# Kernel tuning notes

Hardware: AMD Instinct MI355X
Metric: run time of the kernel (lower is better)

The kernel has to match this reference:

```python
import jax, jax.numpy as jnp
import numpy as np

N_NODES = 100000
N_GRAPHS = 1000
NPG = 100           # nodes per graph (fixed)
N_EDGES = 3200000   # avg degree 32
F_IN = 128
K = 30              # SortAggregation k
N_CLASSES = 10


def setup_inputs() -> dict:
    key = jax.random.key(0)
    ks = jax.random.split(key, 24)
    x = jax.random.normal(ks[0], (N_NODES, F_IN), jnp.float32)
    # edges constrained within each 100-node graph
    g = jax.random.randint(ks[1], (N_EDGES,), 0, N_GRAPHS)
    src = g * NPG + jax.random.randint(ks[2], (N_EDGES,), 0, NPG)
    dst = g * NPG + jax.random.randint(ks[3], (N_EDGES,), 0, NPG)
    edge_index = jnp.stack([src, dst]).astype(jnp.int32)
    batch = jnp.repeat(jnp.arange(N_GRAPHS, dtype=jnp.int32), NPG)

    def lin(k, fi, fo):
        return jax.random.normal(k, (fi, fo), jnp.float32) / np.sqrt(fi)

    return {
        "x": x, "edge_index": edge_index, "batch": batch,
        "W1": lin(ks[4], F_IN, 32), "b1": jnp.zeros((32,), jnp.float32),
        "W2": lin(ks[5], 32, 32),   "b2": jnp.zeros((32,), jnp.float32),
        "W3": lin(ks[6], 32, 32),   "b3": jnp.zeros((32,), jnp.float32),
        "W4": lin(ks[7], 32, 1),    "b4": jnp.zeros((1,), jnp.float32),
        "conv5_w": jax.random.normal(ks[8], (16, 1, 97), jnp.float32) / np.sqrt(97.0),
        "conv5_b": jnp.zeros((16,), jnp.float32),
        "conv6_w": jax.random.normal(ks[9], (32, 16, 5), jnp.float32) / np.sqrt(16 * 5.0),
        "conv6_b": jnp.zeros((32,), jnp.float32),
        "fc1_w": lin(ks[10], 352, 128), "fc1_b": jnp.zeros((128,), jnp.float32),
        "fc2_w": lin(ks[11], 128, N_CLASSES), "fc2_b": jnp.zeros((N_CLASSES,), jnp.float32),
    }


def reference(x, edge_index, batch,
              W1, b1, W2, b2, W3, b3, W4, b4,
              conv5_w, conv5_b, conv6_w, conv6_b,
              fc1_w, fc1_b, fc2_w, fc2_b):
    N = x.shape[0]
    src, dst = edge_index[0], edge_index[1]
    # remove_self_loops -> zero edge weight; GCNConv then re-adds self loops (weight 1)
    w = jnp.where(src == dst, 0.0, 1.0).astype(x.dtype)
    deg = jax.ops.segment_sum(w, dst, num_segments=N) + 1.0  # includes self loop
    dis = jax.lax.rsqrt(deg)
    norm = w * dis[src] * dis[dst]        # per-edge D^-1/2 A D^-1/2
    self_norm = dis * dis                 # self-loop coefficient 1/deg

    def gcn(h, W, b):
        h = h @ W                                   # [N, out]
        agg = jax.ops.segment_sum(norm[:, None] * h[src], dst, num_segments=N)
        return agg + self_norm[:, None] * h + b

    x1 = jnp.tanh(gcn(x, W1, b1))
    x2 = jnp.tanh(gcn(x1, W2, b2))
    x3 = jnp.tanh(gcn(x2, W3, b3))
    x4 = jnp.tanh(gcn(x3, W4, b4))
    h = jnp.concatenate([x1, x2, x3, x4], axis=-1)  # [N, 97]
    C = h.shape[-1]

    # SortAggregation(k=30): per graph, sort nodes by last channel descending, keep top k
    xs = h.reshape(N_GRAPHS, NPG, C)
    order = jnp.argsort(-xs[..., -1], axis=1)[:, :K]            # [B, K]
    pooled = jnp.take_along_axis(xs, order[:, :, None], axis=1)  # [B, K, C]
    y = pooled.reshape(N_GRAPHS, 1, K * C)                       # [B, 1, 2910]

    dn = ('NCH', 'OIH', 'NCH')
    y = jax.lax.conv_general_dilated(y, conv5_w, (97,), 'VALID', dimension_numbers=dn)
    y = jax.nn.relu(y + conv5_b[None, :, None])                  # [B, 16, 30]
    B, Co, L = y.shape
    y = y.reshape(B, Co, L // 2, 2).max(axis=-1)                 # maxpool(2,2) -> [B,16,15]
    y = jax.lax.conv_general_dilated(y, conv6_w, (1,), 'VALID', dimension_numbers=dn)
    y = jax.nn.relu(y + conv6_b[None, :, None])                  # [B, 32, 11]
    y = y.reshape(B, -1)                                         # [B, 352]
    out = jax.nn.relu(y @ fc1_w + fc1_b)                         # dropout = identity (eval)
    return jax.nn.log_softmax(out @ fc2_w + fc2_b, axis=-1)
```

## Files before the change

kernel.cpp:

```cpp
#include <hip/hip_runtime.h>

#define N_GRAPHS_C 1000
#define NPG_C      100
#define N_EDGES_C  3200000
#define KTOP_C     30
#define CAP        4096
#define NB_BUCKET  391

typedef _Float16 f16x8 __attribute__((ext_vector_type(8)));
typedef float    f32x4 __attribute__((ext_vector_type(4)));

__device__ __forceinline__ unsigned packh2(float x, float y) {
    _Float16 hx = (_Float16)x, hy = (_Float16)y;
    return (unsigned)__builtin_bit_cast(unsigned short, hx) |
           ((unsigned)__builtin_bit_cast(unsigned short, hy) << 16);
}

__device__ __forceinline__ float f16b(unsigned v) {
    return (float)__builtin_bit_cast(_Float16, (unsigned short)v);
}

__device__ __forceinline__ float ftanh(float x) {
    float e = __expf(2.0f * x);
    return 1.0f - 2.0f * __builtin_amdgcn_rcpf(e + 1.0f);
}

__device__ __forceinline__ void split8(const float* v, f16x8& h, f16x8& l) {
    #pragma unroll
    for (int j = 0; j < 8; ++j) {
        _Float16 hh = (_Float16)v[j];
        h[j] = hh;
        l[j] = (_Float16)(v[j] - (float)hh);
    }
}


__global__ __launch_bounds__(1024)
void bucket_kernel(const int* __restrict__ src, const int* __restrict__ dst,
                   int* __restrict__ gcur, unsigned short* __restrict__ slots,
                   const float* __restrict__ W1, const float* __restrict__ W2,
                   const float* __restrict__ W3, unsigned* __restrict__ wp) {
    const int tid = threadIdx.x;
    if (blockIdx.x == NB_BUCKET) {
        for (int w = tid; w < 2048; w += 1024) {
            int n = w >> 6, kp = w & 63, k = kp * 2;
            float a = W1[k*32 + n], b = W1[(k+1)*32 + n];
            _Float16 ah = (_Float16)a, bh = (_Float16)b;
            wp[w]        = (unsigned)__builtin_bit_cast(unsigned short, ah) |
                           ((unsigned)__builtin_bit_cast(unsigned short, bh) << 16);
            wp[2048 + w] = packh2(a - (float)ah, b - (float)bh);
        }
        for (int w = tid; w < 512; w += 1024) {
            int n = w >> 4, kp = w & 15, k = kp * 2;
            float a = W2[k*32 + n], b = W2[(k+1)*32 + n];
            _Float16 ah = (_Float16)a, bh = (_Float16)b;
            wp[4096 + w] = (unsigned)__builtin_bit_cast(unsigned short, ah) |
                           ((unsigned)__builtin_bit_cast(unsigned short, bh) << 16);
            wp[4608 + w] = packh2(a - (float)ah, b - (float)bh);
            float a3 = W3[k*32 + n], b3v = W3[(k+1)*32 + n];
            _Float16 a3h = (_Float16)a3, b3h = (_Float16)b3v;
            wp[5120 + w] = (unsigned)__builtin_bit_cast(unsigned short, a3h) |
                           ((unsigned)__builtin_bit_cast(unsigned short, b3h) << 16);
            wp[5632 + w] = packh2(a3 - (float)a3h, b3v - (float)b3h);
        }
        return;
    }

    __shared__ int hist[N_GRAPHS_C];
    const int base = blockIdx.x * 8192;
    for (int i = tid; i < N_GRAPHS_C; i += 1024) hist[i] = 0;
    __syncthreads();

    int g[8]; unsigned short pk[8]; bool v[8];
    #pragma unroll
    for (int k = 0; k < 8; ++k) {
        int e = base + tid + k * 1024;
        v[k] = false;
        if (e < N_EDGES_C) {
            int s = src[e], d = dst[e];
            if (s != d) {
                int gg = s / NPG_C;
                g[k] = gg;
                pk[k] = (unsigned short)(((d - gg * NPG_C) << 7) | (s - gg * NPG_C));
                v[k] = true;
                atomicAdd(&hist[gg], 1);
            }
        }
    }
    __syncthreads();
    for (int i = tid; i < N_GRAPHS_C; i += 1024) {
        int c = hist[i];
        hist[i] = atomicAdd(&gcur[i], c);
    }
    __syncthreads();
    #pragma unroll
    for (int k = 0; k < 8; ++k) {
        if (v[k]) {
            int pos = atomicAdd(&hist[g[k]], 1);
            if (pos < CAP) slots[g[k] * CAP + pos] = pk[k];
        }
    }
}

#define SMEM_WORDS 8496

extern "C" __global__ __launch_bounds__(512, 8)
void dgcnn_kernel(const float* __restrict__ x,
                  const int* __restrict__ gcur, const unsigned short* __restrict__ slots,
                  const unsigned* __restrict__ wp,
                  const float* __restrict__ b1, const float* __restrict__ b2,
                  const float* __restrict__ b3,
                  const float* __restrict__ W4, const float* __restrict__ b4,
                  const float* __restrict__ w5, const float* __restrict__ b5,
                  const float* __restrict__ w6, const float* __restrict__ b6,
                  const float* __restrict__ fw1, const float* __restrict__ fb1,
                  const float* __restrict__ fw2, const float* __restrict__ fb2,
                  float* __restrict__ out)
{
    extern __shared__ unsigned smu[];
    unsigned* planes = smu;
    float* xrows  = (float*)(smu + 4352);
    float* pooled = (float*)(smu + 4352);
    float* dis = (float*)(smu + 7952);
    float* t4  = (float*)(smu + 8064);
    unsigned* t4h = smu + 8168;
    unsigned* t4l = smu + 8232;
    float* sX4 = (float*)(smu + 8296);
    int*   srank = (int*)(smu + 8396);
    float* s5  = (float*)smu;
    float* sPb = s5 + 480;
    float* s6  = s5 + 720;
    float* sO1 = s5 + 1072;
    float* sFc = s5 + 1200;
    float* sZ  = s5 + 1712;

    const int tid = threadIdx.x;
    const int g   = blockIdx.x;
    const int l64 = tid & 63;
    const int wv  = tid >> 6;

    const float* xg = x + (size_t)g * NPG_C * 128;
    const unsigned* w1h = wp;
    const unsigned* w1l = wp + 2048;

    for (int idx = tid; idx < 2600; idx += 512) planes[idx] = 0u;
    if (tid < 12) dis[100 + tid] = 0.f;
    if (tid < 100) srank[tid] = 0;
    __syncthreads();

    {
        int ec = gcur[g]; if (ec > CAP) ec = CAP;
        for (int k = tid; k < ec; k += 512) {
            unsigned e = slots[g * CAP + k];
            unsigned idx = (e >> 7) * 104 + (e & 127);
            atomicAdd(&planes[idx >> 2], 1u << ((idx & 3) * 8));
        }
    }
    __syncthreads();

    if (tid < 400) {
        int row = tid >> 2, part = tid & 3;
        int wb = part * 7, we = (part == 3) ? 26 : wb + 7;
        const unsigned* rw = planes + row * 26;
        unsigned s = 0;
        for (int k = wb; k < we; ++k) {
            unsigned v = rw[k];
            s += (v & 0xffu) + ((v >> 8) & 0xffu) + ((v >> 16) & 0xffu) + (v >> 24);
        }
        atomicAdd(&srank[row], (int)s);
    }
    f16x8 afr[4];
    {
        const int arow = (wv << 4) + (l64 & 15);
        if (wv < 7 && arow < 100) {
            const unsigned* cb = planes + arow * 26 + ((l64 >> 4) << 1);
            #pragma unroll
            for (int ks = 0; ks < 4; ++ks) {
                uint2 cw = *(const uint2*)(cb + ks * 8);
                #pragma unroll
                for (int j = 0; j < 4; ++j) {
                    afr[ks][j]     = (_Float16)(float)((cw.x >> (8*j)) & 255u);
                    afr[ks][4 + j] = (_Float16)(float)((cw.y >> (8*j)) & 255u);
                }
            }
        } else {
            #pragma unroll
            for (int ks = 0; ks < 4; ++ks)
                #pragma unroll
                for (int j = 0; j < 8; ++j) afr[ks][j] = (_Float16)0.f;
        }
    }
    __syncthreads();

    if (tid < 100) dis[tid] = rsqrtf((float)srank[tid] + 1.0f);
    __syncthreads();

    auto packStore = [&](f32x4 c, int n, int r0, float4 dv) {
        float v0 = c[0]*dv.x, v1 = c[1]*dv.y, v2 = c[2]*dv.z, v3 = c[3]*dv.w;
        _Float16 h0=(_Float16)v0, h1=(_Float16)v1, h2=(_Float16)v2, h3=(_Float16)v3;
        uint2 wh, wl;
        wh.x = (unsigned)__builtin_bit_cast(unsigned short,h0) |
               ((unsigned)__builtin_bit_cast(unsigned short,h1) << 16);
        wh.y = (unsigned)__builtin_bit_cast(unsigned short,h2) |
               ((unsigned)__builtin_bit_cast(unsigned short,h3) << 16);
        wl.x = packh2(v0-(float)h0, v1-(float)h1);
        wl.y = packh2(v2-(float)h2, v3-(float)h3);
        *(uint2*)&planes[n*68 + (r0>>1)] = wh;
        *(uint2*)&planes[2176 + n*68 + (r0>>1)] = wl;
    };

    for (int idx = tid; idx < 768; idx += 512) {
        int rw = idx / 12, wd = idx - rw * 12;
        planes[rw * 68 + 56 + wd] = 0u;
    }
    if (wv < 7) {
        f32x4 c0 = {0.f,0.f,0.f,0.f}, c1 = {0.f,0.f,0.f,0.f};
        const int arow = (wv << 4) + (l64 & 15);
        const int kq   = (l64 >> 4) << 3;
        const int bn   = l64 & 15;
        const bool aok = arow < 100;
        #pragma unroll
        for (int kc = 0; kc < 4; ++kc) {
            const int kb = (kc << 5) + kq;
            f16x8 ah, al;
            if (aok) {
                float av[8];
                float4 xa = *(const float4*)&xg[arow*128 + kb];
                float4 xb = *(const float4*)&xg[arow*128 + kb + 4];
                av[0]=xa.x; av[1]=xa.y; av[2]=xa.z; av[3]=xa.w;
                av[4]=xb.x; av[5]=xb.y; av[6]=xb.z; av[7]=xb.w;
                split8(av, ah, al);
            } else {
                #pragma unroll
                for (int j = 0; j < 8; ++j) { ah[j] = (_Float16)0.f; al[j] = (_Float16)0.f; }
            }
            f16x8 b0h = __builtin_bit_cast(f16x8, *(const uint4*)(w1h + bn*64 + (kb>>1)));
            f16x8 b0l = __builtin_bit_cast(f16x8, *(const uint4*)(w1l + bn*64 + (kb>>1)));
            f16x8 b1h = __builtin_bit_cast(f16x8, *(const uint4*)(w1h + (bn+16)*64 + (kb>>1)));
            f16x8 b1l = __builtin_bit_cast(f16x8, *(const uint4*)(w1l + (bn+16)*64 + (kb>>1)));
            c0 = __builtin_amdgcn_mfma_f32_16x16x32_f16(ah, b0h, c0, 0, 0, 0);
            c0 = __builtin_amdgcn_mfma_f32_16x16x32_f16(al, b0h, c0, 0, 0, 0);
            c0 = __builtin_amdgcn_mfma_f32_16x16x32_f16(ah, b0l, c0, 0, 0, 0);
            c1 = __builtin_amdgcn_mfma_f32_16x16x32_f16(ah, b1h, c1, 0, 0, 0);
            c1 = __builtin_amdgcn_mfma_f32_16x16x32_f16(al, b1h, c1, 0, 0, 0);
            c1 = __builtin_amdgcn_mfma_f32_16x16x32_f16(ah, b1l, c1, 0, 0, 0);
        }
        const int r0 = (wv << 4) + ((l64 >> 4) << 2);
        float4 dv = *(const float4*)&dis[r0];
        packStore(c0, bn,      r0, dv);
        packStore(c1, bn + 16, r0, dv);
    }
    __syncthreads();

    auto AGG = [&](f32x4& fa, f32x4& fb, const float* Bp, bool wx) {
        if (wv < 7) {
            f32x4 a0 = {0.f,0.f,0.f,0.f}, a1 = {0.f,0.f,0.f,0.f};
            const unsigned* bb = planes + (l64 & 15) * 68 + ((l64 >> 4) << 2);
            #pragma unroll
            for (int p = 0; p < 2; ++p) {
                const unsigned* bp = bb + p * 2176;
                #pragma unroll
                for (int ks = 0; ks < 4; ++ks) {
                    f16x8 b0 = __builtin_bit_cast(f16x8, *(const uint4*)(bp + ks*16));
                    f16x8 b1 = __builtin_bit_cast(f16x8, *(const uint4*)(bp + 16*68 + ks*16));
                    a0 = __builtin_amdgcn_mfma_f32_16x16x32_f16(afr[ks], b0, a0, 0, 0, 0);
                    a1 = __builtin_amdgcn_mfma_f32_16x16x32_f16(afr[ks], b1, a1, 0, 0, 0);
                }
            }
            int n0 = l64 & 15, r0 = (wv << 4) + ((l64 >> 4) << 2);
            uint2 sh0 = *(const uint2*)(planes + n0 * 68 + (r0 >> 1));
            uint2 sl0 = *(const uint2*)(planes + 2176 + n0 * 68 + (r0 >> 1));
            uint2 sh1 = *(const uint2*)(planes + (16 + n0) * 68 + (r0 >> 1));
            uint2 sl1 = *(const uint2*)(planes + 2176 + (16 + n0) * 68 + (r0 >> 1));
            float4 dv = *(const float4*)&dis[r0];
            float bi0 = Bp[n0], bi1 = Bp[16 + n0];
            #pragma unroll
            for (int j = 0; j < 4; ++j) {
                unsigned sft = (unsigned)((j & 1) * 16);
                float sc0 = f16b(((j < 2) ? sh0.x : sh0.y) >> sft) +
                            f16b(((j < 2) ? sl0.x : sl0.y) >> sft);
                float sc1 = f16b(((j < 2) ? sh1.x : sh1.y) >> sft) +
                            f16b(((j < 2) ? sl1.x : sl1.y) >> sft);
                float d_ = (j == 0) ? dv.x : (j == 1) ? dv.y : (j == 2) ? dv.z : dv.w;
                float v0 = ftanh(d_ * (a0[j] + sc0) + bi0);
                float v1 = ftanh(d_ * (a1[j] + sc1) + bi1);
                fa[j] = v0; fb[j] = v1;
                if (wx) {
                    int row = r0 + j;
                    if (row < 100) { xrows[row*36 + n0] = v0; xrows[row*36 + 16 + n0] = v1; }
                }
            }
        }
    };

    auto XWm = [&](const unsigned* wh, const unsigned* wl) {
        if (wv < 7) {
            f32x4 c0 = {0.f,0.f,0.f,0.f}, c1 = {0.f,0.f,0.f,0.f};
            const int arow = (wv << 4) + (l64 & 15);
            const int kq   = (l64 >> 4) << 3;
            const int bn   = l64 & 15;
            f16x8 ah, al;
            if (arow < 100) {
                float av[8];
                float4 xa = *(const float4*)&xrows[arow*36 + kq];
                float4 xb = *(const float4*)&xrows[arow*36 + kq + 4];
                av[0]=xa.x; av[1]=xa.y; av[2]=xa.z; av[3]=xa.w;
                av[4]=xb.x; av[5]=xb.y; av[6]=xb.z; av[7]=xb.w;
                split8(av, ah, al);
            } else {
                #pragma unroll
                for (int j = 0; j < 8; ++j) { ah[j] = (_Float16)0.f; al[j] = (_Float16)0.f; }
            }
            f16x8 b0h = __builtin_bit_cast(f16x8, *(const uint4*)(wh + bn*16 + (kq>>1)));
            f16x8 b0l = __builtin_bit_cast(f16x8, *(const uint4*)(wl + bn*16 + (kq>>1)));
            f16x8 b1h = __builtin_bit_cast(f16x8, *(const uint4*)(wh + (bn+16)*16 + (kq>>1)));
            f16x8 b1l = __builtin_bit_cast(f16x8, *(const uint4*)(wl + (bn+16)*16 + (kq>>1)));
            c0 = __builtin_amdgcn_mfma_f32_16x16x32_f16(ah, b0h, c0, 0, 0, 0);
            c0 = __builtin_amdgcn_mfma_f32_16x16x32_f16(al, b0h, c0, 0, 0, 0);
            c0 = __builtin_amdgcn_mfma_f32_16x16x32_f16(ah, b0l, c0, 0, 0, 0);
            c1 = __builtin_amdgcn_mfma_f32_16x16x32_f16(ah, b1h, c1, 0, 0, 0);
            c1 = __builtin_amdgcn_mfma_f32_16x16x32_f16(al, b1h, c1, 0, 0, 0);
            c1 = __builtin_amdgcn_mfma_f32_16x16x32_f16(ah, b1l, c1, 0, 0, 0);
            const int r0 = (wv << 4) + ((l64 >> 4) << 2);
            float4 dv = *(const float4*)&dis[r0];
            packStore(c0, bn,      r0, dv);
            packStore(c1, bn + 16, r0, dv);
        }
    };

    f32x4 f1a, f1b, f2a, f2b, f3a, f3b;

    AGG(f1a, f1b, b1, true);        __syncthreads();
    XWm(wp + 4096, wp + 4608);      __syncthreads();
    AGG(f2a, f2b, b2, true);        __syncthreads();
    XWm(wp + 5120, wp + 5632);      __syncthreads();
    AGG(f3a, f3b, b3, false);

    if (wv < 7) {
        float w4a = W4[l64 & 15], w4b = W4[16 + (l64 & 15)];
        int r0 = (wv << 4) + ((l64 >> 4) << 2);
        #pragma unroll
        for (int j = 0; j < 4; ++j) {
            float v = f3a[j] * w4a + f3b[j] * w4b;
            v += __shfl_xor(v, 1, 16); v += __shfl_xor(v, 2, 16);
            v += __shfl_xor(v, 4, 16); v += __shfl_xor(v, 8, 16);
            int row = r0 + j;
            if ((l64 & 15) == 0 && row < 100) t4[row] = v * dis[row];
        }
    }
    __syncthreads();

    if (tid < 64) {
        float a = (2*tid < 100) ? t4[2*tid] : 0.f;
        float b = (2*tid+1 < 100) ? t4[2*tid+1] : 0.f;
        _Float16 ah = (_Float16)a, bh = (_Float16)b;
        t4h[tid] = (unsigned)__builtin_bit_cast(unsigned short, ah) |
                   ((unsigned)__builtin_bit_cast(unsigned short, bh) << 16);
        t4l[tid] = packh2(a - (float)ah, b - (float)bh);
    }
    if (tid < 100) srank[tid] = 0;
    __syncthreads();

    if (wv < 7) {
        f32x4 c = {0.f,0.f,0.f,0.f};
        const int kq2 = (l64 >> 4) << 2;
        const bool bz = (l64 & 15) == 0;
        #pragma unroll
        for (int ks = 0; ks < 4; ++ks) {
            f16x8 bh, bl;
            if (bz) {
                bh = __builtin_bit_cast(f16x8, *(const uint4*)(t4h + ks*16 + kq2));
                bl = __builtin_bit_cast(f16x8, *(const uint4*)(t4l + ks*16 + kq2));
            } else {
                #pragma unroll
                for (int j = 0; j < 8; ++j) { bh[j] = (_Float16)0.f; bl[j] = (_Float16)0.f; }
            }
            c = __builtin_amdgcn_mfma_f32_16x16x32_f16(afr[ks], bh, c, 0, 0, 0);
            c = __builtin_amdgcn_mfma_f32_16x16x32_f16(afr[ks], bl, c, 0, 0, 0);
        }
        if (bz) {
            int r0 = (wv << 4) + ((l64 >> 4) << 2);
            #pragma unroll
            for (int j = 0; j < 4; ++j) {
                int row = r0 + j;
                if (row < 100) sX4[row] = tanhf(dis[row] * (c[j] + t4[row]) + b4[0]);
            }
        }
    }
    __syncthreads();

    if (tid < 500) {
        int i = tid / 5, seg = tid - i * 5;
        float vi = sX4[i];
        int c = 0, jb = seg * 20;
        #pragma unroll
        for (int jo = 0; jo < 20; ++jo) {
            int j = jb + jo;
            float vj = sX4[j];
            c += (vj > vi) || (vj == vi && j < i);
        }
        atomicAdd(&srank[i], c);
    }
    __syncthreads();

    if (wv < 7) {
        int n0 = l64 & 15, r0 = (wv << 4) + ((l64 >> 4) << 2);
        #pragma unroll
        for (int j = 0; j < 4; ++j) {
            int row = r0 + j;
            if (row < 100) {
                int rk = srank[row];
                if (rk < KTOP_C) {
                    float* pr = pooled + rk * 100;
                    pr[n0]      = f1a[j]; pr[16 + n0] = f1b[j];
                    pr[32 + n0] = f2a[j]; pr[48 + n0] = f2b[j];
                    pr[64 + n0] = f3a[j]; pr[80 + n0] = f3b[j];
                    if (n0 == 0) pr[96] = sX4[row];
                }
            }
        }
    }
    __syncthreads();

    if (tid < 480) {
        int l = tid >> 4, co = tid & 15;
        const float* pr = pooled + l * 100;
        const float* wr = w5 + co * 97;
        float acc = b5[co];
        for (int c4 = 0; c4 < 96; c4 += 4) {
            const float4 pv = *(const float4*)&pr[c4];
            acc = fmaf(pv.x, wr[c4+0], fmaf(pv.y, wr[c4+1], fmaf(pv.z, wr[c4+2], fmaf(pv.w, wr[c4+3], acc))));
        }
        acc = fmaf(pr[96], wr[96], acc);
        s5[co * 30 + l] = fmaxf(acc, 0.f);
    }
    __syncthreads();

    if (tid < 240) {
        int co = tid / 15, j = tid - co * 15;
        sPb[co * 15 + j] = fmaxf(s5[co * 30 + 2*j], s5[co * 30 + 2*j + 1]);
    }
    __syncthreads();

    if (tid < 352) {
        int co = tid / 11, l = tid - co * 11;
        float acc = b6[co];
        for (int ci = 0; ci < 16; ++ci) {
            const float* wr = w6 + (co * 16 + ci) * 5;
            const float* pr = sPb + ci * 15 + l;
            acc = fmaf(wr[0], pr[0], fmaf(wr[1], pr[1], fmaf(wr[2], pr[2],
                  fmaf(wr[3], pr[3], fmaf(wr[4], pr[4], acc)))));
        }
        s6[co * 11 + l] = fmaxf(acc, 0.f);
    }
    __syncthreads();

    {
        int j = tid & 127, part = tid >> 7;
        int ibeg = part * 88, iend = ibeg + 88;
        float acc = (part == 0) ? fb1[j] : 0.f;
        for (int i = ibeg; i < iend; ++i)
            acc = fmaf(s6[i], fw1[i * 128 + j], acc);
        sFc[part * 128 + j] = acc;
    }
    __syncthreads();
    if (tid < 128) {
        float v = sFc[tid] + sFc[128 + tid] + sFc[256 + tid] + sFc[384 + tid];
        sO1[tid] = fmaxf(v, 0.f);
    }
    __syncthreads();

    if (tid < 10) {
        float acc = fb2[tid];
        for (int k = 0; k < 128; ++k)
            acc = fmaf(sO1[k], fw2[k * 10 + tid], acc);
        sZ[tid] = acc;
    }
    __syncthreads();
    if (tid < 10) {
        float m = sZ[0];
        for (int c = 1; c < 10; ++c) m = fmaxf(m, sZ[c]);
        float se = 0.f;
        for (int c = 0; c < 10; ++c) se += expf(sZ[c] - m);
        out[g * 10 + tid] = sZ[tid] - m - logf(se);
    }
}

extern "C" void kernel_launch(void* const* d_in, const int* in_sizes, int n_in,
                              void* d_out, int out_size, void* d_ws, size_t ws_size,
                              hipStream_t stream) {
    const float* x   = (const float*)d_in[0];
    const int*   ei  = (const int*)d_in[1];
    const int*   src = ei;
    const int*   dst = ei + N_EDGES_C;
    const float* W1 = (const float*)d_in[3];  const float* b1 = (const float*)d_in[4];
    const float* W2 = (const float*)d_in[5];  const float* b2 = (const float*)d_in[6];
    const float* W3 = (const float*)d_in[7];  const float* b3 = (const float*)d_in[8];
    const float* W4 = (const float*)d_in[9];  const float* b4 = (const float*)d_in[10];
    const float* w5 = (const float*)d_in[11]; const float* b5 = (const float*)d_in[12];
    const float* w6 = (const float*)d_in[13]; const float* b6 = (const float*)d_in[14];
    const float* fw1 = (const float*)d_in[15]; const float* fb1 = (const float*)d_in[16];
    const float* fw2 = (const float*)d_in[17]; const float* fb2 = (const float*)d_in[18];
    float* out = (float*)d_out;

    int* gcur = (int*)d_ws;
    unsigned short* slots = (unsigned short*)((char*)d_ws + 4096);
    unsigned* wpp = (unsigned*)((char*)d_ws + 4096 + (size_t)N_GRAPHS_C * CAP * 2);

    hipMemsetAsync(gcur, 0, 4096, stream);

    bucket_kernel<<<NB_BUCKET + 1, 1024, 0, stream>>>(src, dst, gcur, slots,
                                                      W1, W2, W3, wpp);

    size_t smem = (size_t)SMEM_WORDS * sizeof(unsigned);
    hipFuncSetAttribute((const void*)dgcnn_kernel,
                        hipFuncAttributeMaxDynamicSharedMemorySize, (int)smem);
    dgcnn_kernel<<<N_GRAPHS_C, 512, smem, stream>>>(
        x, gcur, slots, wpp, b1, b2, b3, W4, b4,
        w5, b5, w6, b6, fw1, fb1, fw2, fb2, out);
}
```

Measured before the change: 106.0 us.

## Halve block to 256 threads with two row tiles per wave

The per-graph kernel drops from 512 to 256 threads. Each wave now processes two 16-row MFMA tiles, so the row-tile loops, fragment arrays and accumulator arrays are doubled per thread. The edge counts move into a separate shared region, conv5 and maxpool are fused, and the rank computation becomes one thread per node. The goal is less idle-wave overhead and fewer syncs, and more blocks per CU with less waste. The cost is higher register pressure and longer serial work per thread.

```diff
diff --git a/kernel.cpp b/kernel.cpp
--- a/kernel.cpp
+++ b/kernel.cpp
@@ -104,7 +104,7 @@
 
 #define SMEM_WORDS 8496
 
-extern "C" __global__ __launch_bounds__(512, 8)
+extern "C" __global__ __launch_bounds__(256, 4)
 void dgcnn_kernel(const float* __restrict__ x,
                   const int* __restrict__ gcur, const unsigned short* __restrict__ slots,
                   const unsigned* __restrict__ wp,
@@ -119,6 +119,7 @@
 {
     extern __shared__ unsigned smu[];
     unsigned* planes = smu;
+    unsigned* cnt    = smu + 4352;
     float* xrows  = (float*)(smu + 4352);
     float* pooled = (float*)(smu + 4352);
     float* dis = (float*)(smu + 7952);
@@ -127,12 +128,11 @@
     unsigned* t4l = smu + 8232;
     float* sX4 = (float*)(smu + 8296);
     int*   srank = (int*)(smu + 8396);
-    float* s5  = (float*)smu;
-    float* sPb = s5 + 480;
-    float* s6  = s5 + 720;
-    float* sO1 = s5 + 1072;
-    float* sFc = s5 + 1200;
-    float* sZ  = s5 + 1712;
+    float* sPb = (float*)smu;
+    float* s6  = (float*)smu + 240;
+    float* sO1 = (float*)smu + 592;
+    float* sFc = (float*)smu + 720;
+    float* sZ  = (float*)smu + 976;
 
     const int tid = threadIdx.x;
     const int g   = blockIdx.x;
@@ -143,25 +143,27 @@
     const unsigned* w1h = wp;
     const unsigned* w1l = wp + 2048;
 
-    for (int idx = tid; idx < 2600; idx += 512) planes[idx] = 0u;
+    for (int idx = tid; idx < 2600; idx += 256) cnt[idx] = 0u;
     if (tid < 12) dis[100 + tid] = 0.f;
     if (tid < 100) srank[tid] = 0;
+    if (tid >= 112 && tid < 120) t4h[56 + tid - 112] = 0u;
+    if (tid >= 120 && tid < 128) t4l[56 + tid - 120] = 0u;
     __syncthreads();
 
     {
         int ec = gcur[g]; if (ec > CAP) ec = CAP;
-        for (int k = tid; k < ec; k += 512) {
+        for (int k = tid; k < ec; k += 256) {
             unsigned e = slots[g * CAP + k];
             unsigned idx = (e >> 7) * 104 + (e & 127);
-            atomicAdd(&planes[idx >> 2], 1u << ((idx & 3) * 8));
-        }
-    }
-    __syncthreads();
-
-    if (tid < 400) {
-        int row = tid >> 2, part = tid & 3;
-        int wb = part * 7, we = (part == 3) ? 26 : wb + 7;
-        const unsigned* rw = planes + row * 26;
+            atomicAdd(&cnt[idx >> 2], 1u << ((idx & 3) * 8));
+        }
+    }
+    __syncthreads();
+
+    if (tid < 200) {
+        int row = tid >> 1, part = tid & 1;
+        int wb = part * 13, we = wb + 13;
+        const unsigned* rw = cnt + row * 26;
         unsigned s = 0;
         for (int k = wb; k < we; ++k) {
             unsigned v = rw[k];
@@ -169,25 +171,27 @@
         }
         atomicAdd(&srank[row], (int)s);
     }
-    f16x8 afr[4];
-    {
-        const int arow = (wv << 4) + (l64 & 15);
-        if (wv < 7 && arow < 100) {
-            const unsigned* cb = planes + arow * 26 + ((l64 >> 4) << 1);
+    f16x8 afr[8];
+    #pragma unroll
+    for (int rt = 0; rt < 2; ++rt) {
+        const int ti = 2*wv + rt;
+        const int arow = ti * 16 + (l64 & 15);
+        if (ti < 7 && arow < 100) {
+            const unsigned* cb = cnt + arow * 26 + ((l64 >> 4) << 1);
             #pragma unroll
             for (int ks = 0; ks < 4; ++ks) {
                 uint2 cw = *(const uint2*)(cb + ks * 8);
                 #pragma unroll
                 for (int j = 0; j < 4; ++j) {
-                    afr[ks][j]     = (_Float16)(float)((cw.x >> (8*j)) & 255u);
-                    afr[ks][4 + j] = (_Float16)(float)((cw.y >> (8*j)) & 255u);
+                    afr[rt*4+ks][j]     = (_Float16)(float)((cw.x >> (8*j)) & 255u);
+                    afr[rt*4+ks][4 + j] = (_Float16)(float)((cw.y >> (8*j)) & 255u);
                 }
             }
         } else {
             #pragma unroll
             for (int ks = 0; ks < 4; ++ks)
                 #pragma unroll
-                for (int j = 0; j < 8; ++j) afr[ks][j] = (_Float16)0.f;
+                for (int j = 0; j < 8; ++j) afr[rt*4+ks][j] = (_Float16)0.f;
         }
     }
     __syncthreads();
@@ -209,241 +213,277 @@
         *(uint2*)&planes[2176 + n*68 + (r0>>1)] = wl;
     };
 
-    for (int idx = tid; idx < 768; idx += 512) {
+    for (int idx = tid; idx < 768; idx += 256) {
         int rw = idx / 12, wd = idx - rw * 12;
         planes[rw * 68 + 56 + wd] = 0u;
     }
-    if (wv < 7) {
-        f32x4 c0 = {0.f,0.f,0.f,0.f}, c1 = {0.f,0.f,0.f,0.f};
-        const int arow = (wv << 4) + (l64 & 15);
-        const int kq   = (l64 >> 4) << 3;
-        const int bn   = l64 & 15;
-        const bool aok = arow < 100;
-        #pragma unroll
-        for (int kc = 0; kc < 4; ++kc) {
-            const int kb = (kc << 5) + kq;
-            f16x8 ah, al;
-            if (aok) {
-                float av[8];
-                float4 xa = *(const float4*)&xg[arow*128 + kb];
-                float4 xb = *(const float4*)&xg[arow*128 + kb + 4];
-                av[0]=xa.x; av[1]=xa.y; av[2]=xa.z; av[3]=xa.w;
-                av[4]=xb.x; av[5]=xb.y; av[6]=xb.z; av[7]=xb.w;
-                split8(av, ah, al);
-            } else {
-                #pragma unroll
-                for (int j = 0; j < 8; ++j) { ah[j] = (_Float16)0.f; al[j] = (_Float16)0.f; }
-            }
-            f16x8 b0h = __builtin_bit_cast(f16x8, *(const uint4*)(w1h + bn*64 + (kb>>1)));
-            f16x8 b0l = __builtin_bit_cast(f16x8, *(const uint4*)(w1l + bn*64 + (kb>>1)));
-            f16x8 b1h = __builtin_bit_cast(f16x8, *(const uint4*)(w1h + (bn+16)*64 + (kb>>1)));
-            f16x8 b1l = __builtin_bit_cast(f16x8, *(const uint4*)(w1l + (bn+16)*64 + (kb>>1)));
-            c0 = __builtin_amdgcn_mfma_f32_16x16x32_f16(ah, b0h, c0, 0, 0, 0);
-            c0 = __builtin_amdgcn_mfma_f32_16x16x32_f16(al, b0h, c0, 0, 0, 0);
-            c0 = __builtin_amdgcn_mfma_f32_16x16x32_f16(ah, b0l, c0, 0, 0, 0);
-            c1 = __builtin_amdgcn_mfma_f32_16x16x32_f16(ah, b1h, c1, 0, 0, 0);
-            c1 = __builtin_amdgcn_mfma_f32_16x16x32_f16(al, b1h, c1, 0, 0, 0);
-            c1 = __builtin_amdgcn_mfma_f32_16x16x32_f16(ah, b1l, c1, 0, 0, 0);
-        }
-        const int r0 = (wv << 4) + ((l64 >> 4) << 2);
-        float4 dv = *(const float4*)&dis[r0];
-        packStore(c0, bn,      r0, dv);
-        packStore(c1, bn + 16, r0, dv);
-    }
-    __syncthreads();
-
-    auto AGG = [&](f32x4& fa, f32x4& fb, const float* Bp, bool wx) {
-        if (wv < 7) {
-            f32x4 a0 = {0.f,0.f,0.f,0.f}, a1 = {0.f,0.f,0.f,0.f};
-            const unsigned* bb = planes + (l64 & 15) * 68 + ((l64 >> 4) << 2);
-            #pragma unroll
-            for (int p = 0; p < 2; ++p) {
-                const unsigned* bp = bb + p * 2176;
-                #pragma unroll
-                for (int ks = 0; ks < 4; ++ks) {
-                    f16x8 b0 = __builtin_bit_cast(f16x8, *(const uint4*)(bp + ks*16));
-                    f16x8 b1 = __builtin_bit_cast(f16x8, *(const uint4*)(bp + 16*68 + ks*16));
-                    a0 = __builtin_amdgcn_mfma_f32_16x16x32_f16(afr[ks], b0, a0, 0, 0, 0);
-                    a1 = __builtin_amdgcn_mfma_f32_16x16x32_f16(afr[ks], b1, a1, 0, 0, 0);
-                }
-            }
-            int n0 = l64 & 15, r0 = (wv << 4) + ((l64 >> 4) << 2);
-            uint2 sh0 = *(const uint2*)(planes + n0 * 68 + (r0 >> 1));
-            uint2 sl0 = *(const uint2*)(planes + 2176 + n0 * 68 + (r0 >> 1));
-            uint2 sh1 = *(const uint2*)(planes + (16 + n0) * 68 + (r0 >> 1));
-            uint2 sl1 = *(const uint2*)(planes + 2176 + (16 + n0) * 68 + (r0 >> 1));
-            float4 dv = *(const float4*)&dis[r0];
-            float bi0 = Bp[n0], bi1 = Bp[16 + n0];
-            #pragma unroll
-            for (int j = 0; j < 4; ++j) {
-                unsigned sft = (unsigned)((j & 1) * 16);
-                float sc0 = f16b(((j < 2) ? sh0.x : sh0.y) >> sft) +
-                            f16b(((j < 2) ? sl0.x : sl0.y) >> sft);
-                float sc1 = f16b(((j < 2) ? sh1.x : sh1.y) >> sft) +
-                            f16b(((j < 2) ? sl1.x : sl1.y) >> sft);
-                float d_ = (j == 0) ? dv.x : (j == 1) ? dv.y : (j == 2) ? dv.z : dv.w;
-                float v0 = ftanh(d_ * (a0[j] + sc0) + bi0);
-                float v1 = ftanh(d_ * (a1[j] + sc1) + bi1);
-                fa[j] = v0; fb[j] = v1;
-                if (wx) {
-                    int row = r0 + j;
-                    if (row < 100) { xrows[row*36 + n0] = v0; xrows[row*36 + 16 + n0] = v1; }
-                }
-            }
-        }
-    };
-
-    auto XWm = [&](const unsigned* wh, const unsigned* wl) {
-        if (wv < 7) {
+    if (tid < 100) srank[tid] = 0;
+    #pragma unroll
+    for (int rt = 0; rt < 2; ++rt) {
+        const int ti = 2*wv + rt;
+        if (ti < 7) {
             f32x4 c0 = {0.f,0.f,0.f,0.f}, c1 = {0.f,0.f,0.f,0.f};
-            const int arow = (wv << 4) + (l64 & 15);
+            const int arow = ti * 16 + (l64 & 15);
             const int kq   = (l64 >> 4) << 3;
             const int bn   = l64 & 15;
-            f16x8 ah, al;
-            if (arow < 100) {
-                float av[8];
-                float4 xa = *(const float4*)&xrows[arow*36 + kq];
-                float4 xb = *(const float4*)&xrows[arow*36 + kq + 4];
-                av[0]=xa.x; av[1]=xa.y; av[2]=xa.z; av[3]=xa.w;
-                av[4]=xb.x; av[5]=xb.y; av[6]=xb.z; av[7]=xb.w;
-                split8(av, ah, al);
-            } else {
-                #pragma unroll
-                for (int j = 0; j < 8; ++j) { ah[j] = (_Float16)0.f; al[j] = (_Float16)0.f; }
-            }
-            f16x8 b0h = __builtin_bit_cast(f16x8, *(const uint4*)(wh + bn*16 + (kq>>1)));
-            f16x8 b0l = __builtin_bit_cast(f16x8, *(const uint4*)(wl + bn*16 + (kq>>1)));
-            f16x8 b1h = __builtin_bit_cast(f16x8, *(const uint4*)(wh + (bn+16)*16 + (kq>>1)));
-            f16x8 b1l = __builtin_bit_cast(f16x8, *(const uint4*)(wl + (bn+16)*16 + (kq>>1)));
-            c0 = __builtin_amdgcn_mfma_f32_16x16x32_f16(ah, b0h, c0, 0, 0, 0);
-            c0 = __builtin_amdgcn_mfma_f32_16x16x32_f16(al, b0h, c0, 0, 0, 0);
-            c0 = __builtin_amdgcn_mfma_f32_16x16x32_f16(ah, b0l, c0, 0, 0, 0);
-            c1 = __builtin_amdgcn_mfma_f32_16x16x32_f16(ah, b1h, c1, 0, 0, 0);
-            c1 = __builtin_amdgcn_mfma_f32_16x16x32_f16(al, b1h, c1, 0, 0, 0);
-            c1 = __builtin_amdgcn_mfma_f32_16x16x32_f16(ah, b1l, c1, 0, 0, 0);
-            const int r0 = (wv << 4) + ((l64 >> 4) << 2);
+            const bool aok = arow < 100;
+            #pragma unroll
+            for (int kc = 0; kc < 4; ++kc) {
+                const int kb = (kc << 5) + kq;
+                f16x8 ah, al;
+                if (aok) {
+                    float av[8];
+                    float4 xa = *(const float4*)&xg[arow*128 + kb];
+                    float4 xb = *(const float4*)&xg[arow*128 + kb + 4];
+                    av[0]=xa.x; av[1]=xa.y; av[2]=xa.z; av[3]=xa.w;
+                    av[4]=xb.x; av[5]=xb.y; av[6]=xb.z; av[7]=xb.w;
+                    split8(av, ah, al);
+                } else {
+                    #pragma unroll
+                    for (int j = 0; j < 8; ++j) { ah[j] = (_Float16)0.f; al[j] = (_Float16)0.f; }
+                }
+                f16x8 b0h = __builtin_bit_cast(f16x8, *(const uint4*)(w1h + bn*64 + (kb>>1)));
+                f16x8 b0l = __builtin_bit_cast(f16x8, *(const uint4*)(w1l + bn*64 + (kb>>1)));
+                f16x8 b1h = __builtin_bit_cast(f16x8, *(const uint4*)(w1h + (bn+16)*64 + (kb>>1)));
+                f16x8 b1l = __builtin_bit_cast(f16x8, *(const uint4*)(w1l + (bn+16)*64 + (kb>>1)));
+                c0 = __builtin_amdgcn_mfma_f32_16x16x32_f16(ah, b0h, c0, 0, 0, 0);
+                c0 = __builtin_amdgcn_mfma_f32_16x16x32_f16(al, b0h, c0, 0, 0, 0);
+                c0 = __builtin_amdgcn_mfma_f32_16x16x32_f16(ah, b0l, c0, 0, 0, 0);
+                c1 = __builtin_amdgcn_mfma_f32_16x16x32_f16(ah, b1h, c1, 0, 0, 0);
+                c1 = __builtin_amdgcn_mfma_f32_16x16x32_f16(al, b1h, c1, 0, 0, 0);
+                c1 = __builtin_amdgcn_mfma_f32_16x16x32_f16(ah, b1l, c1, 0, 0, 0);
+            }
+            const int r0 = ti * 16 + ((l64 >> 4) << 2);
             float4 dv = *(const float4*)&dis[r0];
             packStore(c0, bn,      r0, dv);
             packStore(c1, bn + 16, r0, dv);
         }
+    }
+    __syncthreads();
+
+    auto AGG = [&](f32x4* fa, f32x4* fb, const float* Bp, bool wx) {
+        #pragma unroll
+        for (int rt = 0; rt < 2; ++rt) {
+            const int ti = 2*wv + rt;
+            if (ti < 7) {
+                f32x4 a0 = {0.f,0.f,0.f,0.f}, a1 = {0.f,0.f,0.f,0.f};
+                const unsigned* bb = planes + (l64 & 15) * 68 + ((l64 >> 4) << 2);
+                #pragma unroll
+                for (int p = 0; p < 2; ++p) {
+                    const unsigned* bp = bb + p * 2176;
+                    #pragma unroll
+                    for (int ks = 0; ks < 4; ++ks) {
+                        f16x8 b0 = __builtin_bit_cast(f16x8, *(const uint4*)(bp + ks*16));
+                        f16x8 b1 = __builtin_bit_cast(f16x8, *(const uint4*)(bp + 16*68 + ks*16));
+                        a0 = __builtin_amdgcn_mfma_f32_16x16x32_f16(afr[rt*4+ks], b0, a0, 0, 0, 0);
+                        a1 = __builtin_amdgcn_mfma_f32_16x16x32_f16(afr[rt*4+ks], b1, a1, 0, 0, 0);
+                    }
+                }
+                int n0 = l64 & 15, r0 = ti * 16 + ((l64 >> 4) << 2);
+                uint2 sh0 = *(const uint2*)(planes + n0 * 68 + (r0 >> 1));
+                uint2 sl0 = *(const uint2*)(planes + 2176 + n0 * 68 + (r0 >> 1));
+                uint2 sh1 = *(const uint2*)(planes + (16 + n0) * 68 + (r0 >> 1));
+                uint2 sl1 = *(const uint2*)(planes + 2176 + (16 + n0) * 68 + (r0 >> 1));
+                float4 dv = *(const float4*)&dis[r0];
+                float bi0 = Bp[n0], bi1 = Bp[16 + n0];
+                #pragma unroll
+                for (int j = 0; j < 4; ++j) {
+                    unsigned sft = (unsigned)((j & 1) * 16);
+                    float sc0 = f16b(((j < 2) ? sh0.x : sh0.y) >> sft) +
+                                f16b(((j < 2) ? sl0.x : sl0.y) >> sft);
+                    float sc1 = f16b(((j < 2) ? sh1.x : sh1.y) >> sft) +
+                                f16b(((j < 2) ? sl1.x : sl1.y) >> sft);
+                    float d_ = (j == 0) ? dv.x : (j == 1) ? dv.y : (j == 2) ? dv.z : dv.w;
+                    float v0 = ftanh(d_ * (a0[j] + sc0) + bi0);
+                    float v1 = ftanh(d_ * (a1[j] + sc1) + bi1);
+                    fa[rt][j] = v0; fb[rt][j] = v1;
+                    if (wx) {
+                        int row = r0 + j;
+                        if (row < 100) { xrows[row*36 + n0] = v0; xrows[row*36 + 16 + n0] = v1; }
+                    }
+                }
+            }
+        }
     };
 
-    f32x4 f1a, f1b, f2a, f2b, f3a, f3b;
-
-    AGG(f1a, f1b, b1, true);        __syncthreads();
-    XWm(wp + 4096, wp + 4608);      __syncthreads();
-    AGG(f2a, f2b, b2, true);        __syncthreads();
-    XWm(wp + 5120, wp + 5632);      __syncthreads();
+    auto XWm = [&](const unsigned* wh, const unsigned* wl) {
+        #pragma unroll
+        for (int rt = 0; rt < 2; ++rt) {
+            const int ti = 2*wv + rt;
+            if (ti < 7) {
+                f32x4 c0 = {0.f,0.f,0.f,0.f}, c1 = {0.f,0.f,0.f,0.f};
+                const int arow = ti * 16 + (l64 & 15);
+                const int kq   = (l64 >> 4) << 3;
+                const int bn   = l64 & 15;
+                f16x8 ah, al;
+                if (arow < 100) {
+                    float av[8];
+                    float4 xa = *(const float4*)&xrows[arow*36 + kq];
+                    float4 xb = *(const float4*)&xrows[arow*36 + kq + 4];
+                    av[0]=xa.x; av[1]=xa.y; av[2]=xa.z; av[3]=xa.w;
+                    av[4]=xb.x; av[5]=xb.y; av[6]=xb.z; av[7]=xb.w;
+                    split8(av, ah, al);
+                } else {
+                    #pragma unroll
+                    for (int j = 0; j < 8; ++j) { ah[j] = (_Float16)0.f; al[j] = (_Float16)0.f; }
+                }
+                f16x8 b0h = __builtin_bit_cast(f16x8, *(const uint4*)(wh + bn*16 + (kq>>1)));
+                f16x8 b0l = __builtin_bit_cast(f16x8, *(const uint4*)(wl + bn*16 + (kq>>1)));
+                f16x8 b1h = __builtin_bit_cast(f16x8, *(const uint4*)(wh + (bn+16)*16 + (kq>>1)));
+                f16x8 b1l = __builtin_bit_cast(f16x8, *(const uint4*)(wl + (bn+16)*16 + (kq>>1)));
+                c0 = __builtin_amdgcn_mfma_f32_16x16x32_f16(ah, b0h, c0, 0, 0, 0);
+                c0 = __builtin_amdgcn_mfma_f32_16x16x32_f16(al, b0h, c0, 0, 0, 0);
+                c0 = __builtin_amdgcn_mfma_f32_16x16x32_f16(ah, b0l, c0, 0, 0, 0);
+                c1 = __builtin_amdgcn_mfma_f32_16x16x32_f16(ah, b1h, c1, 0, 0, 0);
+                c1 = __builtin_amdgcn_mfma_f32_16x16x32_f16(al, b1h, c1, 0, 0, 0);
+                c1 = __builtin_amdgcn_mfma_f32_16x16x32_f16(ah, b1l, c1, 0, 0, 0);
+                const int r0 = ti * 16 + ((l64 >> 4) << 2);
+                float4 dv = *(const float4*)&dis[r0];
+                packStore(c0, bn,      r0, dv);
+                packStore(c1, bn + 16, r0, dv);
+            }
+        }
+    };
+
+    f32x4 f1a[2], f1b[2], f2a[2], f2b[2], f3a[2], f3b[2];
+
+    AGG(f1a, f1b, b1, true);
+    __syncthreads();
+    XWm(wp + 4096, wp + 4608);
+    __syncthreads();
+    AGG(f2a, f2b, b2, true);
+    __syncthreads();
+    XWm(wp + 5120, wp + 5632);
+    __syncthreads();
     AGG(f3a, f3b, b3, false);
 
-    if (wv < 7) {
+    {
         float w4a = W4[l64 & 15], w4b = W4[16 + (l64 & 15)];
-        int r0 = (wv << 4) + ((l64 >> 4) << 2);
         #pragma unroll
-        for (int j = 0; j < 4; ++j) {
-            float v = f3a[j] * w4a + f3b[j] * w4b;
-            v += __shfl_xor(v, 1, 16); v += __shfl_xor(v, 2, 16);
-            v += __shfl_xor(v, 4, 16); v += __shfl_xor(v, 8, 16);
-            int row = r0 + j;
-            if ((l64 & 15) == 0 && row < 100) t4[row] = v * dis[row];
-        }
-    }
-    __syncthreads();
-
-    if (tid < 64) {
-        float a = (2*tid < 100) ? t4[2*tid] : 0.f;
-        float b = (2*tid+1 < 100) ? t4[2*tid+1] : 0.f;
-        _Float16 ah = (_Float16)a, bh = (_Float16)b;
-        t4h[tid] = (unsigned)__builtin_bit_cast(unsigned short, ah) |
-                   ((unsigned)__builtin_bit_cast(unsigned short, bh) << 16);
-        t4l[tid] = packh2(a - (float)ah, b - (float)bh);
-    }
-    if (tid < 100) srank[tid] = 0;
-    __syncthreads();
-
-    if (wv < 7) {
-        f32x4 c = {0.f,0.f,0.f,0.f};
+        for (int rt = 0; rt < 2; ++rt) {
+            const int ti = 2*wv + rt;
+            if (ti < 7) {
+                int r0 = ti * 16 + ((l64 >> 4) << 2);
+                float tv[4];
+                #pragma unroll
+                for (int j = 0; j < 4; ++j) {
+                    float v = f3a[rt][j] * w4a + f3b[rt][j] * w4b;
+                    v += __shfl_xor(v, 1, 16); v += __shfl_xor(v, 2, 16);
+                    v += __shfl_xor(v, 4, 16); v += __shfl_xor(v, 8, 16);
+                    int row = r0 + j;
+                    tv[j] = (row < 100) ? v * dis[row] : 0.f;
+                }
+                if ((l64 & 15) == 0) {
+                    #pragma unroll
+                    for (int j = 0; j < 4; ++j) { int row = r0 + j; if (row < 100) t4[row] = tv[j]; }
+                    _Float16 h0=(_Float16)tv[0], h1=(_Float16)tv[1];
+                    _Float16 h2=(_Float16)tv[2], h3=(_Float16)tv[3];
+                    uint2 wh, wl;
+                    wh.x = (unsigned)__builtin_bit_cast(unsigned short,h0) |
+                           ((unsigned)__builtin_bit_cast(unsigned short,h1) << 16);
+                    wh.y = (unsigned)__builtin_bit_cast(unsigned short,h2) |
+                           ((unsigned)__builtin_bit_cast(unsigned short,h3) << 16);
+                    wl.x = packh2(tv[0]-(float)h0, tv[1]-(float)h1);
+                    wl.y = packh2(tv[2]-(float)h2, tv[3]-(float)h3);
+                    *(uint2*)&t4h[r0 >> 1] = wh;
+                    *(uint2*)&t4l[r0 >> 1] = wl;
+                }
+            }
+        }
+    }
+    __syncthreads();
+
+    {
         const int kq2 = (l64 >> 4) << 2;
         const bool bz = (l64 & 15) == 0;
         #pragma unroll
-        for (int ks = 0; ks < 4; ++ks) {
-            f16x8 bh, bl;
-            if (bz) {
-                bh = __builtin_bit_cast(f16x8, *(const uint4*)(t4h + ks*16 + kq2));
-                bl = __builtin_bit_cast(f16x8, *(const uint4*)(t4l + ks*16 + kq2));
-            } else {
-                #pragma unroll
-                for (int j = 0; j < 8; ++j) { bh[j] = (_Float16)0.f; bl[j] = (_Float16)0.f; }
-            }
-            c = __builtin_amdgcn_mfma_f32_16x16x32_f16(afr[ks], bh, c, 0, 0, 0);
-            c = __builtin_amdgcn_mfma_f32_16x16x32_f16(afr[ks], bl, c, 0, 0, 0);
-        }
-        if (bz) {
-            int r0 = (wv << 4) + ((l64 >> 4) << 2);
-            #pragma unroll
-            for (int j = 0; j < 4; ++j) {
-                int row = r0 + j;
-                if (row < 100) sX4[row] = tanhf(dis[row] * (c[j] + t4[row]) + b4[0]);
-            }
-        }
-    }
-    __syncthreads();
-
-    if (tid < 500) {
-        int i = tid / 5, seg = tid - i * 5;
-        float vi = sX4[i];
-        int c = 0, jb = seg * 20;
+        for (int rt = 0; rt < 2; ++rt) {
+            const int ti = 2*wv + rt;
+            if (ti < 7) {
+                f32x4 c = {0.f,0.f,0.f,0.f};
+                #pragma unroll
+                for (int ks = 0; ks < 4; ++ks) {
+                    f16x8 bh, bl;
+                    if (bz) {
+                        bh = __builtin_bit_cast(f16x8, *(const uint4*)(t4h + ks*16 + kq2));
+                        bl = __builtin_bit_cast(f16x8, *(const uint4*)(t4l + ks*16 + kq2));
+                    } else {
+                        #pragma unroll
+                        for (int j = 0; j < 8; ++j) { bh[j] = (_Float16)0.f; bl[j] = (_Float16)0.f; }
+                    }
+                    c = __builtin_amdgcn_mfma_f32_16x16x32_f16(afr[rt*4+ks], bh, c, 0, 0, 0);
+                    c = __builtin_amdgcn_mfma_f32_16x16x32_f16(afr[rt*4+ks], bl, c, 0, 0, 0);
+                }
+                if (bz) {
+                    int r0 = ti * 16 + ((l64 >> 4) << 2);
+                    #pragma unroll
+                    for (int j = 0; j < 4; ++j) {
+                        int row = r0 + j;
+                        if (row < 100) sX4[row] = tanhf(dis[row] * (c[j] + t4[row]) + b4[0]);
+                    }
+                }
+            }
+        }
+    }
+    __syncthreads();
+
+    if (tid < 100) {
+        float vi = sX4[tid];
+        int c = 0;
+        for (int j = 0; j < 100; ++j) {
+            float vj = sX4[j];
+            c += (vj > vi) || (vj == vi && j < tid);
+        }
+        srank[tid] = c;
+    }
+    __syncthreads();
+
+    {
+        int n0 = l64 & 15;
         #pragma unroll
-        for (int jo = 0; jo < 20; ++jo) {
-            int j = jb + jo;
-            float vj = sX4[j];
-            c += (vj > vi) || (vj == vi && j < i);
-        }
-        atomicAdd(&srank[i], c);
-    }
-    __syncthreads();
-
-    if (wv < 7) {
-        int n0 = l64 & 15, r0 = (wv << 4) + ((l64 >> 4) << 2);
+        for (int rt = 0; rt < 2; ++rt) {
+            const int ti = 2*wv + rt;
+            if (ti < 7) {
+                int r0 = ti * 16 + ((l64 >> 4) << 2);
+                #pragma unroll
+                for (int j = 0; j < 4; ++j) {
+                    int row = r0 + j;
+                    if (row < 100) {
+                        int rk = srank[row];
+                        if (rk < KTOP_C) {
+                            float* pr = pooled + rk * 100;
+                            pr[n0]      = f1a[rt][j]; pr[16 + n0] = f1b[rt][j];
+                            pr[32 + n0] = f2a[rt][j]; pr[48 + n0] = f2b[rt][j];
+                            pr[64 + n0] = f3a[rt][j]; pr[80 + n0] = f3b[rt][j];
+                            if (n0 == 0) pr[96] = sX4[row];
+                        }
+                    }
+                }
+            }
+        }
+    }
+    __syncthreads();
+
+    if (tid < 240) {
+        int l2 = tid >> 4, co = tid & 15;
+        const float* wr = w5 + co * 97;
+        float accs[2];
         #pragma unroll
-        for (int j = 0; j < 4; ++j) {
-            int row = r0 + j;
-            if (row < 100) {
-                int rk = srank[row];
-                if (rk < KTOP_C) {
-                    float* pr = pooled + rk * 100;
-                    pr[n0]      = f1a[j]; pr[16 + n0] = f1b[j];
-                    pr[32 + n0] = f2a[j]; pr[48 + n0] = f2b[j];
-                    pr[64 + n0] = f3a[j]; pr[80 + n0] = f3b[j];
-                    if (n0 == 0) pr[96] = sX4[row];
-                }
-            }
-        }
-    }
-    __syncthreads();
-
-    if (tid < 480) {
-        int l = tid >> 4, co = tid & 15;
-        const float* pr = pooled + l * 100;
-        const float* wr = w5 + co * 97;
-        float acc = b5[co];
-        for (int c4 = 0; c4 < 96; c4 += 4) {
-            const float4 pv = *(const float4*)&pr[c4];
-            acc = fmaf(pv.x, wr[c4+0], fmaf(pv.y, wr[c4+1], fmaf(pv.z, wr[c4+2], fmaf(pv.w, wr[c4+3], acc))));
-        }
-        acc = fmaf(pr[96], wr[96], acc);
-        s5[co * 30 + l] = fmaxf(acc, 0.f);
-    }
-    __syncthreads();
-
-    if (tid < 240) {
-        int co = tid / 15, j = tid - co * 15;
-        sPb[co * 15 + j] = fmaxf(s5[co * 30 + 2*j], s5[co * 30 + 2*j + 1]);
-    }
-    __syncthreads();
-
-    if (tid < 352) {
-        int co = tid / 11, l = tid - co * 11;
+        for (int t = 0; t < 2; ++t) {
+            const float* pr = pooled + (2*l2 + t) * 100;
+            float acc = b5[co];
+            for (int c4 = 0; c4 < 96; c4 += 4) {
+                const float4 pv = *(const float4*)&pr[c4];
+                acc = fmaf(pv.x, wr[c4+0], fmaf(pv.y, wr[c4+1], fmaf(pv.z, wr[c4+2], fmaf(pv.w, wr[c4+3], acc))));
+            }
+            accs[t] = fmaf(pr[96], wr[96], acc);
+        }
+        sPb[co * 15 + l2] = fmaxf(fmaxf(accs[0], accs[1]), 0.f);
+    }
+    __syncthreads();
+
+    for (int o = tid; o < 352; o += 256) {
+        int co = o / 11, l = o - co * 11;
         float acc = b6[co];
         for (int ci = 0; ci < 16; ++ci) {
             const float* wr = w6 + (co * 16 + ci) * 5;
@@ -457,7 +497,7 @@
 
     {
         int j = tid & 127, part = tid >> 7;
-        int ibeg = part * 88, iend = ibeg + 88;
+        int ibeg = part * 176, iend = ibeg + 176;
         float acc = (part == 0) ? fb1[j] : 0.f;
         for (int i = ibeg; i < iend; ++i)
             acc = fmaf(s6[i], fw1[i * 128 + j], acc);
@@ -465,7 +505,7 @@
     }
     __syncthreads();
     if (tid < 128) {
-        float v = sFc[tid] + sFc[128 + tid] + sFc[256 + tid] + sFc[384 + tid];
+        float v = sFc[tid] + sFc[128 + tid];
         sO1[tid] = fmaxf(v, 0.f);
     }
     __syncthreads();
@@ -515,7 +555,7 @@
     size_t smem = (size_t)SMEM_WORDS * sizeof(unsigned);
     hipFuncSetAttribute((const void*)dgcnn_kernel,
                         hipFuncAttributeMaxDynamicSharedMemorySize, (int)smem);
-    dgcnn_kernel<<<N_GRAPHS_C, 512, smem, stream>>>(
+    dgcnn_kernel<<<N_GRAPHS_C, 256, smem, stream>>>(
         x, gcur, slots, wpp, b1, b2, b3, W4, b4,
         w5, b5, w6, b6, fw1, fb1, fw2, fb2, out);
 }
```

After: 100.2 us. 5.5% less time.
